# Optimization experiments

Measured on AMD Instinct MI355X. Metric: run time of the kernel, lower is better.

Reference implementation:

```python
import jax, jax.numpy as jnp
import numpy as np

N, T, H, L, E, F, CN, CG = 20000, 2, 128, 4, 320000, 514, 3, 2
EPS = 1e-7  # GENConv message epsilon


def _ln(x, g, b):
    mu = jnp.mean(x, axis=-1, keepdims=True)
    var = jnp.mean((x - mu) ** 2, axis=-1, keepdims=True)
    return (x - mu) / jnp.sqrt(var + 1e-5) * g + b


def _genconv(x, src, dst, e, W1, b1, g1, be1, W2, b2, t, n):
    # message: relu(x_j + edge_attr) + eps
    msg = jax.nn.relu(x[src] + e) + EPS  # [E,H]
    # softmax aggregation with learnable temperature t, grouped by dst
    logits = msg * t
    m = jax.ops.segment_max(logits, dst, num_segments=n)
    m = jnp.where(jnp.isfinite(m), m, 0.0)  # guard empty segments
    ex = jnp.exp(logits - m[dst])
    denom = jax.ops.segment_sum(ex, dst, num_segments=n)
    alpha = ex / (denom[dst] + 1e-16)
    agg = jax.ops.segment_sum(msg * alpha, dst, num_segments=n)  # [N,H]
    out = agg + x  # residual with root node (x_r)
    # MLP: Lin(H,2H) -> LayerNorm -> ReLU -> Lin(2H,H)
    h1 = jax.nn.relu(_ln(out @ W1 + b1, g1, be1))
    return h1 @ W2 + b2


def _attn(x, Wq, Wk, Wv, gamma):
    # x: [N, T, H]; channel (transform-axis) self-attention, gamma-gated residual
    q = jnp.einsum('tc,nch->nth', Wq, x)
    k = jnp.einsum('tc,nch->nth', Wk, x)
    v = jnp.einsum('tc,nch->nth', Wv, x)
    a = jax.nn.softmax(jnp.einsum('nth,nsh->nts', q, k), axis=-1)
    o = jnp.einsum('nts,nsh->nth', a, v)
    return gamma * o + x


def setup_inputs() -> dict:
    key = jax.random.key(0)
    ks = iter(jax.random.split(key, 48))

    def nrm(sh, s=0.02):
        return jax.random.normal(next(ks), sh, dtype=jnp.float32) * s

    inp = {}
    inp['node_feature'] = jax.random.normal(next(ks), (N, F), dtype=jnp.float32)
    inp['edge_index'] = jax.random.randint(next(ks), (T, 2, E), 0, N, dtype=jnp.int32)
    inp['edge_attr'] = jax.random.normal(next(ks), (T, E, 2), dtype=jnp.float32)
    # encoders
    inp['Wne'] = nrm((F, H)); inp['bne'] = jnp.zeros((H,), jnp.float32)
    inp['Wee'] = nrm((2, H)); inp['bee'] = jnp.zeros((H,), jnp.float32)
    # per-layer GENConv MLP params (stacked over L)
    inp['W1'] = nrm((L, H, 2 * H)); inp['b1'] = jnp.zeros((L, 2 * H), jnp.float32)
    inp['g1'] = jnp.ones((L, 2 * H), jnp.float32); inp['be1'] = jnp.zeros((L, 2 * H), jnp.float32)
    inp['W2'] = nrm((L, 2 * H, H)); inp['b2'] = jnp.zeros((L, H), jnp.float32)
    # DeepGCNLayer LayerNorms
    inp['dg'] = jnp.ones((L, H), jnp.float32); inp['db'] = jnp.zeros((L, H), jnp.float32)
    # learnable temperatures
    inp['t'] = jnp.ones((L,), jnp.float32)
    # node attention + head
    inp['Wq_n'] = nrm((T, T), 0.2); inp['Wk_n'] = nrm((T, T), 0.2); inp['Wv_n'] = nrm((T, T), 0.2)
    inp['gamma_n'] = jnp.float32(0.5)
    inp['Wn1'] = nrm((T * H, T * H)); inp['bn1'] = jnp.zeros((T * H,), jnp.float32)
    inp['Wn2'] = nrm((T * H, CN)); inp['bn2'] = jnp.zeros((CN,), jnp.float32)
    # graph attention + head
    inp['Wq_g'] = nrm((T, T), 0.2); inp['Wk_g'] = nrm((T, T), 0.2); inp['Wv_g'] = nrm((T, T), 0.2)
    inp['gamma_g'] = jnp.float32(0.5)
    inp['Wg1'] = nrm((T * H, T * H)); inp['bg1'] = jnp.zeros((T * H,), jnp.float32)
    inp['Wg2'] = nrm((T * H, CG)); inp['bg2'] = jnp.zeros((CG,), jnp.float32)
    return inp


def reference(node_feature, edge_index, edge_attr, Wne, bne, Wee, bee,
              W1, b1, g1, be1, W2, b2, dg, db, t,
              Wq_n, Wk_n, Wv_n, gamma_n, Wn1, bn1, Wn2, bn2,
              Wq_g, Wk_g, Wv_g, gamma_g, Wg1, bg1, Wg2, bg2):
    embs = []
    for ti in range(T):
        x = node_feature @ Wne + bne           # node_encoder
        e = edge_attr[ti] @ Wee + bee          # edge_encoder
        src, dst = edge_index[ti, 0], edge_index[ti, 1]
        # layers[0].conv applied directly
        x = _genconv(x, src, dst, e, W1[0], b1[0], g1[0], be1[0], W2[0], b2[0], t[0], N)
        # res+ DeepGCN blocks
        for l in range(1, L):
            h = jax.nn.relu(_ln(x, dg[l], db[l]))  # dropout p=0.1 is identity in eval
            x = x + _genconv(h, src, dst, e, W1[l], b1[l], g1[l], be1[l], W2[l], b2[l], t[l], N)
        x = jax.nn.relu(_ln(x, dg[0], db[0]))
        embs.append(x)
    emb = jnp.stack(embs, axis=1)  # [N, T, H]

    a = _attn(emb, Wq_n, Wk_n, Wv_n, gamma_n).reshape(N, T * H)
    node = jax.nn.relu(a @ Wn1 + bn1) @ Wn2 + bn2
    node = jax.nn.log_softmax(node, axis=-1)

    g = _attn(emb, Wq_g, Wk_g, Wv_g, gamma_g).reshape(N, T * H)
    gp = jnp.mean(g, axis=0, keepdims=True)  # global_mean_pool (single graph)
    gp = jax.nn.relu(gp @ Wg1 + bg1) @ Wg2 + bg2
    gp = jax.nn.log_softmax(gp, axis=-1)
    return (node, gp)
```

## Files before the change

kernel.cpp:

```cpp
#include <hip/hip_runtime.h>

#define NN 20000
#define TT 2
#define HH 128
#define LL 4
#define EE 320000
#define FF 514
#define CN 3
#define CG 2
#define EPS_MSG 1e-7f
#define MP 20096

typedef __bf16 bf16x8 __attribute__((ext_vector_type(8)));
typedef __bf16 bf16x4 __attribute__((ext_vector_type(4)));
typedef __bf16 bf16x2 __attribute__((ext_vector_type(2)));
typedef float f32x4 __attribute__((ext_vector_type(4)));

struct __align__(8) Edge { int src; __bf16 ea0, ea1; };

__device__ inline float wave_sum(float v) {
#pragma unroll
  for (int off = 32; off; off >>= 1) v += __shfl_xor(v, off);
  return v;
}
__device__ inline float red16(float v) {
  v += __shfl_xor(v, 1); v += __shfl_xor(v, 2);
  v += __shfl_xor(v, 4); v += __shfl_xor(v, 8);
  return v;
}

__device__ __forceinline__ void gload_lds16(const void* g, void* l) {
  __builtin_amdgcn_global_load_lds(
      (const __attribute__((address_space(1))) unsigned int*)g,
      (__attribute__((address_space(3))) unsigned int*)l, 16, 0, 0);
}

#define ENCB (MP / 64)
#define SCB 2500
#define CHUNK 5000
__global__ __launch_bounds__(256) void enc_scatter_kernel(
    const __bf16* __restrict__ A, const __bf16* __restrict__ BT,
    const float* __restrict__ bias, __bf16* __restrict__ C,
    const int* __restrict__ edge_index, const float* __restrict__ edge_attr,
    int* __restrict__ cursor, Edge* __restrict__ edges) {
  __shared__ __bf16 As[2][64][32];
  __shared__ __bf16 Bs[2][128][32];
  const int tid = threadIdx.x;
  if (blockIdx.x >= ENCB) {
    int chunk = blockIdx.x & 7;
    int i = ((blockIdx.x - ENCB) >> 3) * 256 + tid;
    if (i >= 2 * EE) return;
    int ti = (i >= EE) ? 1 : 0;
    int e = i - ti * EE;
    const int* srcp = edge_index + (size_t)ti * 2 * EE;
    int d = srcp[EE + e];
    int gnode = ti * NN + d;
    if (gnode / CHUNK != chunk) return;
    int s = srcp[e];
    float2 ea = ((const float2*)edge_attr)[(size_t)ti * EE + e];
    int pos = atomicAdd(&cursor[gnode], 1);
    Edge ed;
    ed.src = s + ti * MP;
    ed.ea0 = (__bf16)ea.x; ed.ea1 = (__bf16)ea.y;
    __builtin_memcpy(&edges[pos], &ed, sizeof(Edge));
    return;
  }
  const int K = 576;
  const int lane = tid & 63, w = tid >> 6;
  const int bm = blockIdx.x * 64;
  const int wr = (w >> 1) * 32, wc = (w & 1) * 64;
  const int fr = lane & 15, fq = lane >> 4;
  const int rowA = tid >> 2, chA = (tid & 3) * 8;
  const __bf16* Ab = A + (size_t)(bm + rowA) * K + chA;
  const __bf16* Bb = BT + (size_t)rowA * K + chA;
  const __bf16* Bb2 = Bb + (size_t)64 * K;
  f32x4 acc[2][4] = {};
#define STAGE(buf, k0)                                  \
  do {                                                  \
    gload_lds16(Ab + (k0), &As[buf][rowA][chA]);        \
    gload_lds16(Bb + (k0), &Bs[buf][rowA][chA]);        \
    gload_lds16(Bb2 + (k0), &Bs[buf][rowA + 64][chA]);  \
  } while (0)
  STAGE(0, 0);
  __syncthreads();
  int cur = 0;
  for (int k0 = 0; k0 < K; k0 += 32) {
    if (k0 + 32 < K) STAGE(cur ^ 1, k0 + 32);
    bf16x8 af[2], bq[4];
#pragma unroll
    for (int m = 0; m < 2; ++m)
      af[m] = *(const bf16x8*)&As[cur][wr + m * 16 + fr][fq * 8];
#pragma unroll
    for (int n = 0; n < 4; ++n)
      bq[n] = *(const bf16x8*)&Bs[cur][wc + n * 16 + fr][fq * 8];
#pragma unroll
    for (int m = 0; m < 2; ++m)
#pragma unroll
      for (int n = 0; n < 4; ++n)
        acc[m][n] =
            __builtin_amdgcn_mfma_f32_16x16x32_bf16(af[m], bq[n], acc[m][n], 0, 0, 0);
    __syncthreads();
    cur ^= 1;
  }
#undef STAGE
#pragma unroll
  for (int m = 0; m < 2; ++m) {
#pragma unroll
    for (int n = 0; n < 4; ++n) {
#pragma unroll
      for (int j = 0; j < 4; ++j) {
        int gm = bm + wr + m * 16 + fq * 4 + j;
        int gn = wc + n * 16 + fr;
        if (gm < NN) {
          __bf16 c = (__bf16)(acc[m][n][j] + bias[gn]);
          C[(size_t)gm * 128 + gn] = c;
          C[(size_t)(gm + MP) * 128 + gn] = c;
        }
      }
    }
  }
}

template <int EPI>
__global__ __launch_bounds__(256) void gemm256(
    const __bf16* __restrict__ A, const __bf16* __restrict__ BT,
    const float* __restrict__ bias, const float* __restrict__ g,
    const float* __restrict__ be, const float* __restrict__ W2h,
    const float* __restrict__ b2h, void* __restrict__ outp, int M, int K) {
  __shared__ __bf16 As[2][64][32];
  __shared__ __bf16 Bs[2][256][32];
  const int tid = threadIdx.x;
  const int lane = tid & 63, w = tid >> 6;
  const int bm = blockIdx.x * 64;
  const int wr = w * 16;
  const int fr = lane & 15, fq = lane >> 4;
  const int rowA = tid >> 2, chA = (tid & 3) * 8;
  const __bf16* Ab = A + (size_t)(bm + rowA) * K + chA;
  const __bf16* Bb = BT + (size_t)rowA * K + chA;
  f32x4 acc[16] = {};

#define STG(buf, k0)                                                \
  do {                                                              \
    gload_lds16(Ab + (k0), &As[buf][rowA][chA]);                    \
    _Pragma("unroll") for (int r = 0; r < 4; ++r)                   \
        gload_lds16(Bb + (size_t)(r * 64) * K + (k0),               \
                    &Bs[buf][rowA + r * 64][chA]);                  \
  } while (0)

  STG(0, 0);
  __syncthreads();
  int cur = 0;
  for (int k0 = 0; k0 < K; k0 += 32) {
    if (k0 + 32 < K) STG(cur ^ 1, k0 + 32);
    bf16x8 af = *(const bf16x8*)&As[cur][wr + fr][fq * 8];
#pragma unroll
    for (int n = 0; n < 16; ++n) {
      bf16x8 bq = *(const bf16x8*)&Bs[cur][n * 16 + fr][fq * 8];
      acc[n] = __builtin_amdgcn_mfma_f32_16x16x32_bf16(af, bq, acc[n], 0, 0, 0);
    }
    __syncthreads();
    cur ^= 1;
  }
#undef STG

  float cb[16];
#pragma unroll
  for (int n = 0; n < 16; ++n) cb[n] = bias[n * 16 + fr];

  if constexpr (EPI == 0) {
    float gv[16], bev[16];
#pragma unroll
    for (int n = 0; n < 16; ++n) {
      gv[n] = g[n * 16 + fr];
      bev[n] = be[n * 16 + fr];
    }
    __bf16* outb = (__bf16*)outp;
#pragma unroll
    for (int j = 0; j < 4; ++j) {
      float cj[16], s = 0.f, s2 = 0.f;
#pragma unroll
      for (int n = 0; n < 16; ++n) {
        float c = acc[n][j] + cb[n];
        cj[n] = c; s += c; s2 += c * c;
      }
      s = red16(s); s2 = red16(s2);
      float mu = s * (1.f / 256);
      float var = fmaxf(s2 * (1.f / 256) - mu * mu, 0.f);
      float rr = rsqrtf(var + 1e-5f);
      int gm = bm + wr + fq * 4 + j;
      __bf16* op = outb + (size_t)gm * 256;
#pragma unroll
      for (int n = 0; n < 16; ++n) {
        float y = (cj[n] - mu) * rr * gv[n] + bev[n];
        op[n * 16 + fr] = (__bf16)fmaxf(y, 0.f);
      }
    }
  } else {
    float w0[16], w1[16], w2[16];
#pragma unroll
    for (int n = 0; n < 16; ++n) {
      int col = n * 16 + fr;
      w0[n] = W2h[col * 3 + 0];
      w1[n] = W2h[col * 3 + 1];
      w2[n] = W2h[col * 3 + 2];
    }
    float* outf = (float*)outp;
#pragma unroll
    for (int j = 0; j < 4; ++j) {
      float p0 = 0.f, p1 = 0.f, p2 = 0.f;
#pragma unroll
      for (int n = 0; n < 16; ++n) {
        float h = fmaxf(acc[n][j] + cb[n], 0.f);
        p0 += h * w0[n]; p1 += h * w1[n]; p2 += h * w2[n];
      }
      p0 = red16(p0); p1 = red16(p1); p2 = red16(p2);
      int gm = bm + wr + fq * 4 + j;
      if (fr == 0 && gm < M) {
        float l0 = p0 + b2h[0], l1 = p1 + b2h[1], l2 = p2 + b2h[2];
        float m = fmaxf(l0, fmaxf(l1, l2));
        float lse = m + logf(__expf(l0 - m) + __expf(l1 - m) + __expf(l2 - m));
        outf[(size_t)gm * 3 + 0] = l0 - lse;
        outf[(size_t)gm * 3 + 1] = l1 - lse;
        outf[(size_t)gm * 3 + 2] = l2 - lse;
      }
    }
  }
}

template <int MODE>
__global__ __launch_bounds__(256) void gemm_lin2(
    const __bf16* __restrict__ A, const __bf16* __restrict__ BT,
    const float* __restrict__ bias, float* __restrict__ xres,
    const float* __restrict__ g, const float* __restrict__ be,
    void* __restrict__ lnout) {
  __shared__ __bf16 As[2][64][32];
  __shared__ __bf16 Bs[2][128][32];
  __shared__ float redS[64][2], redS2[64][2];
  const int tid = threadIdx.x;
  const int lane = tid & 63, w = tid >> 6;
  const int bm = blockIdx.x * 64;
  const int wr = (w >> 1) * 32, wc = (w & 1) * 64;
  const int fr = lane & 15, fq = lane >> 4;
  const int rowA = tid >> 2, chA = (tid & 3) * 8;
  const __bf16* Ab = A + (size_t)(bm + rowA) * 256 + chA;
  const __bf16* Bb = BT + (size_t)rowA * 256 + chA;
  const __bf16* Bb2 = Bb + (size_t)64 * 256;
  f32x4 acc[2][4] = {};

#define STAGE(buf, k0)                                  \
  do {                                                  \
    gload_lds16(Ab + (k0), &As[buf][rowA][chA]);        \
    gload_lds16(Bb + (k0), &Bs[buf][rowA][chA]);        \
    gload_lds16(Bb2 + (k0), &Bs[buf][rowA + 64][chA]);  \
  } while (0)

  STAGE(0, 0);
  __syncthreads();
  int cur = 0;
  for (int k0 = 0; k0 < 256; k0 += 32) {
    if (k0 + 32 < 256) STAGE(cur ^ 1, k0 + 32);
    bf16x8 af[2], bq[4];
#pragma unroll
    for (int m = 0; m < 2; ++m)
      af[m] = *(const bf16x8*)&As[cur][wr + m * 16 + fr][fq * 8];
#pragma unroll
    for (int n = 0; n < 4; ++n)
      bq[n] = *(const bf16x8*)&Bs[cur][wc + n * 16 + fr][fq * 8];
#pragma unroll
    for (int m = 0; m < 2; ++m)
#pragma unroll
      for (int n = 0; n < 4; ++n)
        acc[m][n] =
            __builtin_amdgcn_mfma_f32_16x16x32_bf16(af[m], bq[n], acc[m][n], 0, 0, 0);
    __syncthreads();
    cur ^= 1;
  }
#undef STAGE

  float cv[2][4][4];
#pragma unroll
  for (int m = 0; m < 2; ++m) {
    int r0 = wr + m * 16 + fq * 4;
#pragma unroll
    for (int j = 0; j < 4; ++j) {
      int gm = bm + r0 + j;
      float s = 0.f, s2 = 0.f;
#pragma unroll
      for (int n = 0; n < 4; ++n) {
        float c = acc[m][n][j] + bias[wc + n * 16 + fr];
        if (MODE != 0) c += xres[(size_t)gm * 128 + wc + n * 16 + fr];
        cv[m][n][j] = c;
        s += c; s2 += c * c;
      }
      s = red16(s); s2 = red16(s2);
      if (fr == 0) {
        redS[r0 + j][w & 1] = s;
        redS2[r0 + j][w & 1] = s2;
      }
    }
  }
  __syncthreads();
#pragma unroll
  for (int m = 0; m < 2; ++m) {
    int r0 = wr + m * 16 + fq * 4;
#pragma unroll
    for (int j = 0; j < 4; ++j) {
      int r = r0 + j;
      int gm = bm + r;
      float S = redS[r][0] + redS[r][1];
      float S2 = redS2[r][0] + redS2[r][1];
      float mu = S * (1.f / 128);
      float var = fmaxf(S2 * (1.f / 128) - mu * mu, 0.f);
      float rr = rsqrtf(var + 1e-5f);
      if constexpr (MODE < 2) {
        float* xp = xres + (size_t)gm * 128;
        __bf16* hp = (__bf16*)lnout + (size_t)gm * 128;
#pragma unroll
        for (int n = 0; n < 4; ++n) {
          int col = wc + n * 16 + fr;
          float c = cv[m][n][j];
          xp[col] = c;
          float y = (c - mu) * rr * g[col] + be[col];
          hp[col] = (__bf16)fmaxf(y, 0.f);
        }
      } else {
        int half = gm >= MP;
        int node = gm - half * MP;
        if (node < NN) {
          float* ep = (float*)lnout + (size_t)node * 256 + half * 128;
#pragma unroll
          for (int n = 0; n < 4; ++n) {
            int col = wc + n * 16 + fr;
            float y = (cv[m][n][j] - mu) * rr * g[col] + be[col];
            ep[col] = fmaxf(y, 0.f);
          }
        }
      }
    }
  }
}

struct WtDesc { const float* src; __bf16* dst; int K, N, Kpad; };
struct WtDescs { WtDesc d[10]; };
#define NF2B 20079
#define PADB 2422
#define WTB 2880
#define CNTB 2500

__global__ void prep_kernel(const float* __restrict__ nf_src,
                            __bf16* __restrict__ nf_dst, WtDescs descs,
                            const int* __restrict__ edge_index,
                            int* __restrict__ deg, float* __restrict__ gp_sum) {
  int b = blockIdx.x, tid = threadIdx.x;
  if (b < NF2B) {
    int i = b * 256 + tid;
    if (i >= NN * FF / 2) return;
    int row = i / 257;
    int col = (i - row * 257) * 2;
    float2 v = ((const float2*)nf_src)[i];
    bf16x2 o; o[0] = (__bf16)v.x; o[1] = (__bf16)v.y;
    *(bf16x2*)(nf_dst + (size_t)row * 576 + col) = o;
  } else if (b < NF2B + PADB) {
    int i = (b - NF2B) * 256 + tid;
    if (i >= NN * 31) return;
    int row = i / 31, j = i - row * 31;
    bf16x2 z; z[0] = (__bf16)0.f; z[1] = (__bf16)0.f;
    *(bf16x2*)(nf_dst + (size_t)row * 576 + 514 + 2 * j) = z;
  } else if (b < NF2B + PADB + WTB) {
    int wb = b - NF2B - PADB;
    WtDesc de = descs.d[wb / 288];
    int idx = (wb % 288) * 256 + tid;
    if (idx >= de.N * de.Kpad) return;
    int n = idx / de.Kpad, k = idx - n * de.Kpad;
    float v = (k < de.K) ? de.src[(size_t)k * de.N + n] : 0.f;
    de.dst[idx] = (__bf16)v;
  } else if (b < NF2B + PADB + WTB + CNTB) {
    int i = (b - NF2B - PADB - WTB) * 256 + tid;
    if (i >= 2 * EE) return;
    int ti = (i >= EE) ? 1 : 0;
    int e = i - ti * EE;
    int d = edge_index[(size_t)ti * 2 * EE + EE + e];
    atomicAdd(&deg[ti * NN + d], 1);
  } else {
    gp_sum[tid] = 0.f;
  }
}

__global__ __launch_bounds__(1024) void scan2_kernel(
    const int* __restrict__ deg_all, int* __restrict__ rowptr,
    int* __restrict__ cursor) {
  const int ti = blockIdx.x;
  const int* deg = deg_all + ti * NN;
  __shared__ int sums[1024];
  int tid = threadIdx.x;
  int chunk = (NN + 1023) / 1024;
  int begin = tid * chunk, end = min(begin + chunk, NN);
  int s = 0;
  for (int i = begin; i < end; ++i) s += deg[i];
  sums[tid] = s;
  __syncthreads();
  for (int off = 1; off < 1024; off <<= 1) {
    int v = (tid >= off) ? sums[tid - off] : 0;
    __syncthreads();
    sums[tid] += v;
    __syncthreads();
  }
  int running = ti * EE + sums[tid] - s;
  for (int i = begin; i < end; ++i) {
    rowptr[ti * NN + i] = running;
    cursor[ti * NN + i] = running;
    running += deg[i];
  }
  if (tid == 0 && ti == 1) rowptr[2 * NN] = 2 * EE;
}

__global__ __launch_bounds__(256) void agg_kernel(
    const __bf16* __restrict__ xin, const int* __restrict__ rowptr,
    const Edge* __restrict__ edges, const float* __restrict__ Wee,
    const float* __restrict__ bee, const float* __restrict__ tptr, int layer,
    __bf16* __restrict__ out) {
  int wave = threadIdx.x >> 6, lane = threadIdx.x & 63;
  int b = blockIdx.x;
  int h8 = b & 7;
  int half = h8 >> 2;
  int within = (b >> 3) * 4 + (h8 & 3);
  int node = within * 4 + wave;
  int gnode = half * NN + node;
  int xrow = half * MP + node;
  float t = tptr[layer];
  int hh = lane >> 5, c32 = lane & 31, c0 = c32 * 4;
  float w0[4], w1[4], bv[4];
#pragma unroll
  for (int i = 0; i < 4; ++i) {
    w0[i] = Wee[c0 + i];
    w1[i] = Wee[HH + c0 + i];
    bv[i] = bee[c0 + i];
  }
  float den[4] = {}, num[4] = {};
  int e = rowptr[gnode], e1 = rowptr[gnode + 1];

#define MLP4(XV, ED)                                                \
  do {                                                              \
    float eax = (float)(ED).ea0, eay = (float)(ED).ea1;             \
    _Pragma("unroll") for (int i = 0; i < 4; ++i) {                 \
      float m = (float)(XV)[i] + eax * w0[i] + eay * w1[i] + bv[i]; \
      m = fmaxf(m, 0.f) + EPS_MSG;                                  \
      float ex = __expf(m * t);                                     \
      den[i] += ex; num[i] += m * ex;                               \
    }                                                               \
  } while (0)

  for (; e + 8 <= e1; e += 8) {
    Edge E0 = edges[e + hh], E1 = edges[e + 2 + hh];
    Edge E2 = edges[e + 4 + hh], E3 = edges[e + 6 + hh];
    bf16x4 x0 = *(const bf16x4*)(xin + (size_t)E0.src * HH + c0);
    bf16x4 x1 = *(const bf16x4*)(xin + (size_t)E1.src * HH + c0);
    bf16x4 x2 = *(const bf16x4*)(xin + (size_t)E2.src * HH + c0);
    bf16x4 x3 = *(const bf16x4*)(xin + (size_t)E3.src * HH + c0);
    MLP4(x0, E0); MLP4(x1, E1); MLP4(x2, E2); MLP4(x3, E3);
  }
  if (e + 4 <= e1) {
    Edge E0 = edges[e + hh], E1 = edges[e + 2 + hh];
    bf16x4 x0 = *(const bf16x4*)(xin + (size_t)E0.src * HH + c0);
    bf16x4 x1 = *(const bf16x4*)(xin + (size_t)E1.src * HH + c0);
    MLP4(x0, E0); MLP4(x1, E1);
    e += 4;
  }
  if (e + hh < e1) {
    Edge Ea = edges[e + hh];
    bf16x4 xa = *(const bf16x4*)(xin + (size_t)Ea.src * HH + c0);
    MLP4(xa, Ea);
  }
  if (e + 2 + hh < e1) {
    Edge Ea = edges[e + 2 + hh];
    bf16x4 xa = *(const bf16x4*)(xin + (size_t)Ea.src * HH + c0);
    MLP4(xa, Ea);
  }
#undef MLP4

#pragma unroll
  for (int i = 0; i < 4; ++i) {
    den[i] += __shfl_xor(den[i], 32);
    num[i] += __shfl_xor(num[i], 32);
  }
  if (hh == 0) {
    bf16x4 xr = *(const bf16x4*)(xin + (size_t)xrow * HH + c0);
    bf16x4 o;
#pragma unroll
    for (int i = 0; i < 4; ++i)
      o[i] = (__bf16)(num[i] / (den[i] + 1e-16f) + (float)xr[i]);
    *(bf16x4*)(out + (size_t)xrow * HH + c0) = o;
  }
}

__global__ __launch_bounds__(256) void attn2_kernel(
    const float* __restrict__ emb, const float* __restrict__ Wq_n,
    const float* __restrict__ Wk_n, const float* __restrict__ Wv_n,
    const float* __restrict__ gn, const float* __restrict__ Wq_g,
    const float* __restrict__ Wk_g, const float* __restrict__ Wv_g,
    const float* __restrict__ gg, __bf16* __restrict__ outn,
    float* __restrict__ outg, int nNodes) {
  int wave = threadIdx.x >> 6, lane = threadIdx.x & 63;
  int n = blockIdx.x * 4 + wave;
  if (n >= nNodes) return;
  int c0 = lane * 2;
  const float* base = emb + (size_t)n * (2 * HH);
  float2 x0 = *(const float2*)(base + c0);
  float2 x1 = *(const float2*)(base + HH + c0);

#define ATTN_BODY(Wq, Wk, Wv, GAM, O0A, O0B, O1A, O1B)                        \
  {                                                                           \
    float gamma = *(GAM);                                                     \
    float wq00 = Wq[0], wq01 = Wq[1], wq10 = Wq[2], wq11 = Wq[3];             \
    float wk00 = Wk[0], wk01 = Wk[1], wk10 = Wk[2], wk11 = Wk[3];             \
    float wv00 = Wv[0], wv01 = Wv[1], wv10 = Wv[2], wv11 = Wv[3];             \
    float q0a = wq00 * x0.x + wq01 * x1.x, q0b = wq00 * x0.y + wq01 * x1.y;   \
    float q1a = wq10 * x0.x + wq11 * x1.x, q1b = wq10 * x0.y + wq11 * x1.y;   \
    float k0a = wk00 * x0.x + wk01 * x1.x, k0b = wk00 * x0.y + wk01 * x1.y;   \
    float k1a = wk10 * x0.x + wk11 * x1.x, k1b = wk10 * x0.y + wk11 * x1.y;   \
    float v0a = wv00 * x0.x + wv01 * x1.x, v0b = wv00 * x0.y + wv01 * x1.y;   \
    float v1a = wv10 * x0.x + wv11 * x1.x, v1b = wv10 * x0.y + wv11 * x1.y;   \
    float s00 = wave_sum(q0a * k0a + q0b * k0b);                              \
    float s01 = wave_sum(q0a * k1a + q0b * k1b);                              \
    float s10 = wave_sum(q1a * k0a + q1b * k0b);                              \
    float s11 = wave_sum(q1a * k1a + q1b * k1b);                              \
    float m0 = fmaxf(s00, s01);                                               \
    float e00 = __expf(s00 - m0), e01 = __expf(s01 - m0);                     \
    float i0 = 1.f / (e00 + e01);                                             \
    float a00 = e00 * i0, a01 = e01 * i0;                                     \
    float m1 = fmaxf(s10, s11);                                               \
    float e10 = __expf(s10 - m1), e11 = __expf(s11 - m1);                     \
    float i1 = 1.f / (e10 + e11);                                             \
    float a10 = e10 * i1, a11 = e11 * i1;                                     \
    O0A = gamma * (a00 * v0a + a01 * v1a) + x0.x;                             \
    O0B = gamma * (a00 * v0b + a01 * v1b) + x0.y;                             \
    O1A = gamma * (a10 * v0a + a11 * v1a) + x1.x;                             \
    O1B = gamma * (a10 * v0b + a11 * v1b) + x1.y;                             \
  }

  float n0a, n0b, n1a, n1b;
  ATTN_BODY(Wq_n, Wk_n, Wv_n, gn, n0a, n0b, n1a, n1b);
  __bf16* opn = outn + (size_t)n * (2 * HH);
  bf16x2 t0; t0[0] = (__bf16)n0a; t0[1] = (__bf16)n0b;
  bf16x2 t1; t1[0] = (__bf16)n1a; t1[1] = (__bf16)n1b;
  *(bf16x2*)(opn + c0) = t0;
  *(bf16x2*)(opn + HH + c0) = t1;

  float g0a, g0b, g1a, g1b;
  ATTN_BODY(Wq_g, Wk_g, Wv_g, gg, g0a, g0b, g1a, g1b);
  float* opg = outg + (size_t)n * (2 * HH);
  *(float2*)(opg + c0) = make_float2(g0a, g0b);
  *(float2*)(opg + HH + c0) = make_float2(g1a, g1b);
#undef ATTN_BODY
}

__global__ __launch_bounds__(256) void pool_kernel(const float* __restrict__ gbuf,
                                                   float* __restrict__ gp_sum, int nNodes) {
  int c = threadIdx.x;
  float s = 0.f;
  for (int r = blockIdx.x; r < nNodes; r += gridDim.x) s += gbuf[(size_t)r * 256 + c];
  atomicAdd(&gp_sum[c], s);
}

__global__ __launch_bounds__(256) void graph_head_kernel(
    const float* __restrict__ gp_sum, const float* __restrict__ Wg1,
    const float* __restrict__ bg1, const float* __restrict__ Wg2,
    const float* __restrict__ bg2, float* __restrict__ outp, float invN) {
  __shared__ float gp[256];
  __shared__ float h1[256];
  __shared__ float lg[2];
  int tid = threadIdx.x;
  gp[tid] = gp_sum[tid] * invN;
  __syncthreads();
  float acc = bg1[tid];
  for (int k = 0; k < 256; ++k) acc += gp[k] * Wg1[k * 256 + tid];
  h1[tid] = fmaxf(acc, 0.f);
  __syncthreads();
  if (tid < 2) {
    float l = bg2[tid];
    for (int c = 0; c < 256; ++c) l += h1[c] * Wg2[c * 2 + tid];
    lg[tid] = l;
  }
  __syncthreads();
  if (tid == 0) {
    float m = fmaxf(lg[0], lg[1]);
    float lse = m + logf(__expf(lg[0] - m) + __expf(lg[1] - m));
    outp[0] = lg[0] - lse;
    outp[1] = lg[1] - lse;
  }
}

extern "C" void kernel_launch(void* const* d_in, const int* in_sizes, int n_in,
                              void* d_out, int out_size, void* d_ws, size_t ws_size,
                              hipStream_t stream) {
  (void)in_sizes; (void)n_in; (void)out_size; (void)ws_size;
  const float* node_feature = (const float*)d_in[0];
  const int* edge_index = (const int*)d_in[1];
  const float* edge_attr = (const float*)d_in[2];
  const float* Wne = (const float*)d_in[3];
  const float* bne = (const float*)d_in[4];
  const float* Wee = (const float*)d_in[5];
  const float* bee = (const float*)d_in[6];
  const float* W1 = (const float*)d_in[7];
  const float* b1 = (const float*)d_in[8];
  const float* g1 = (const float*)d_in[9];
  const float* be1 = (const float*)d_in[10];
  const float* W2 = (const float*)d_in[11];
  const float* b2 = (const float*)d_in[12];
  const float* dg = (const float*)d_in[13];
  const float* db = (const float*)d_in[14];
  const float* tpar = (const float*)d_in[15];
  const float* Wq_n = (const float*)d_in[16];
  const float* Wk_n = (const float*)d_in[17];
  const float* Wv_n = (const float*)d_in[18];
  const float* gamma_n = (const float*)d_in[19];
  const float* Wn1 = (const float*)d_in[20];
  const float* bn1 = (const float*)d_in[21];
  const float* Wn2 = (const float*)d_in[22];
  const float* bn2 = (const float*)d_in[23];
  const float* Wq_g = (const float*)d_in[24];
  const float* Wk_g = (const float*)d_in[25];
  const float* Wv_g = (const float*)d_in[26];
  const float* gamma_g = (const float*)d_in[27];
  const float* Wg1 = (const float*)d_in[28];
  const float* bg1 = (const float*)d_in[29];
  const float* Wg2 = (const float*)d_in[30];
  const float* bg2 = (const float*)d_in[31];
  float* out = (float*)d_out;

  char* pc = (char*)d_ws;
  auto alloc = [&](size_t bytes) {
    char* r = pc;
    pc += (bytes + 255) & ~(size_t)255;
    return r;
  };
  float* xbuf = (float*)alloc((size_t)2 * MP * HH * 4);
  __bf16* hbuf_b = (__bf16*)alloc((size_t)2 * MP * HH * 2);
  __bf16* t256_b = (__bf16*)alloc((size_t)2 * MP * 256 * 2);
  float* emb = (float*)alloc((size_t)NN * 2 * HH * 4);
  __bf16* aggout_b = (__bf16*)alloc((size_t)2 * MP * HH * 2);
  __bf16* nf_b = (__bf16*)emb;
  __bf16* attnb = t256_b;
  float* buf2 = xbuf;
  __bf16* wt_ne = (__bf16*)alloc((size_t)128 * 576 * 2);
  __bf16* wt1 = (__bf16*)alloc((size_t)4 * 256 * 128 * 2);
  __bf16* wt2 = (__bf16*)alloc((size_t)4 * 128 * 256 * 2);
  __bf16* wtn1 = (__bf16*)alloc((size_t)256 * 256 * 2);
  float* gp_sum = (float*)alloc(256 * 4);
  int* deg = (int*)alloc((size_t)2 * NN * 4);
  int* cursor = (int*)alloc((size_t)2 * NN * 4);
  int* rowptr = (int*)alloc((size_t)(2 * NN + 2) * 4);
  Edge* edges = (Edge*)alloc((size_t)2 * EE * 8);

  const int gRows2 = 2 * MP / 64;

  WtDescs wd;
  wd.d[0] = {Wne, wt_ne, FF, HH, 576};
  for (int l = 0; l < 4; ++l)
    wd.d[1 + l] = {W1 + (size_t)l * HH * 256, wt1 + (size_t)l * 256 * HH, HH, 256, HH};
  for (int l = 0; l < 4; ++l)
    wd.d[5 + l] = {W2 + (size_t)l * 256 * HH, wt2 + (size_t)l * HH * 256, 256, HH, 256};
  wd.d[9] = {Wn1, wtn1, 256, 256, 256};

  hipMemsetAsync(deg, 0, 2 * NN * sizeof(int), stream);
  prep_kernel<<<NF2B + PADB + WTB + CNTB + 1, 256, 0, stream>>>(
      node_feature, nf_b, wd, edge_index, deg, gp_sum);
  scan2_kernel<<<2, 1024, 0, stream>>>(deg, rowptr, cursor);
  enc_scatter_kernel<<<ENCB + 8 * SCB, 256, 0, stream>>>(
      nf_b, wt_ne, bne, hbuf_b, edge_index, edge_attr, cursor, edges);

  for (int l = 0; l < LL; ++l) {
    agg_kernel<<<2 * NN / 4, 256, 0, stream>>>(hbuf_b, rowptr, edges, Wee, bee, tpar,
                                               l, aggout_b);
    gemm256<0><<<gRows2, 256, 0, stream>>>(aggout_b, wt1 + (size_t)l * 256 * HH,
                                           b1 + l * 2 * HH, g1 + l * 2 * HH,
                                           be1 + l * 2 * HH, nullptr, nullptr, t256_b,
                                           2 * MP, HH);
    const __bf16* w2l = wt2 + (size_t)l * HH * 256;
    const float* b2l = b2 + l * HH;
    if (l == 0)
      gemm_lin2<0><<<gRows2, 256, 0, stream>>>(t256_b, w2l, b2l, xbuf, dg + 1 * HH,
                                               db + 1 * HH, hbuf_b);
    else if (l < LL - 1)
      gemm_lin2<1><<<gRows2, 256, 0, stream>>>(t256_b, w2l, b2l, xbuf,
                                               dg + (l + 1) * HH, db + (l + 1) * HH,
                                               hbuf_b);
    else
      gemm_lin2<2><<<gRows2, 256, 0, stream>>>(t256_b, w2l, b2l, xbuf, dg, db, emb);
  }

  attn2_kernel<<<(NN + 3) / 4, 256, 0, stream>>>(emb, Wq_n, Wk_n, Wv_n, gamma_n,
                                                 Wq_g, Wk_g, Wv_g, gamma_g, attnb,
                                                 buf2, NN);
  gemm256<1><<<MP / 64, 256, 0, stream>>>(attnb, wtn1, bn1, nullptr, nullptr, Wn2,
                                          bn2, out, NN, 256);
  pool_kernel<<<128, 256, 0, stream>>>(buf2, gp_sum, NN);
  graph_head_kernel<<<1, 256, 0, stream>>>(gp_sum, Wg1, bg1, Wg2, bg2,
                                           out + (size_t)NN * CN, 1.0f / NN);
}
```

Baseline: 511.8 us.

## Split agg channels across blocks, use exp2, pre-reduce graph pool in attention

The aggregation kernel now gives each block one half of the 128 channels of its node. Each wave covers 64 channels with 16 lanes and handles 4 edges at a time, which doubles the grid and the number of wave-level edge loads. The softmax exponential switches to a native exp2 with the temperature pre-scaled by log2(e). The attention kernel also reduces the graph-branch output over each block's 4 nodes in LDS and writes only per-block partial sums, so the full per-node float buffer is never written and pool_kernel reads a quarter of the rows. The cost is more edge-index reads, since each edge list is walked by two blocks, and the removed bounds check relies on NN being divisible by 4.

```diff
diff --git a/kernel.cpp b/kernel.cpp
--- a/kernel.cpp
+++ b/kernel.cpp
@@ -27,6 +27,14 @@
   v += __shfl_xor(v, 1); v += __shfl_xor(v, 2);
   v += __shfl_xor(v, 4); v += __shfl_xor(v, 8);
   return v;
+}
+
+__device__ __forceinline__ float fexp2(float x) {
+#if __has_builtin(__builtin_amdgcn_exp2f)
+  return __builtin_amdgcn_exp2f(x);
+#else
+  return exp2f(x);
+#endif
 }
 
 __device__ __forceinline__ void gload_lds16(const void* g, void* l) {
@@ -421,14 +429,17 @@
     __bf16* __restrict__ out) {
   int wave = threadIdx.x >> 6, lane = threadIdx.x & 63;
   int b = blockIdx.x;
-  int h8 = b & 7;
-  int half = h8 >> 2;
-  int within = (b >> 3) * 4 + (h8 & 3);
-  int node = within * 4 + wave;
-  int gnode = half * NN + node;
-  int xrow = half * MP + node;
-  float t = tptr[layer];
-  int hh = lane >> 5, c32 = lane & 31, c0 = c32 * 4;
+  int x8 = b & 7;
+  int q = x8 >> 1;
+  int par = x8 & 1;
+  int ti = q >> 1, chh = q & 1;
+  int group = (b >> 3) * 2 + par;
+  int node = group * 4 + wave;
+  int gnode = ti * NN + node;
+  int xrow = ti * MP + node;
+  float t2 = tptr[layer] * 1.4426950408889634f;
+  int qq = lane >> 4, c15 = lane & 15;
+  int c0 = chh * 64 + c15 * 4;
   float w0[4], w1[4], bv[4];
 #pragma unroll
   for (int i = 0; i < 4; ++i) {
@@ -445,45 +456,39 @@
     _Pragma("unroll") for (int i = 0; i < 4; ++i) {                 \
       float m = (float)(XV)[i] + eax * w0[i] + eay * w1[i] + bv[i]; \
       m = fmaxf(m, 0.f) + EPS_MSG;                                  \
-      float ex = __expf(m * t);                                     \
+      float ex = fexp2(m * t2);                                     \
       den[i] += ex; num[i] += m * ex;                               \
     }                                                               \
   } while (0)
 
   for (; e + 8 <= e1; e += 8) {
-    Edge E0 = edges[e + hh], E1 = edges[e + 2 + hh];
-    Edge E2 = edges[e + 4 + hh], E3 = edges[e + 6 + hh];
+    Edge E0 = edges[e + qq];
+    Edge E1 = edges[e + 4 + qq];
     bf16x4 x0 = *(const bf16x4*)(xin + (size_t)E0.src * HH + c0);
     bf16x4 x1 = *(const bf16x4*)(xin + (size_t)E1.src * HH + c0);
-    bf16x4 x2 = *(const bf16x4*)(xin + (size_t)E2.src * HH + c0);
-    bf16x4 x3 = *(const bf16x4*)(xin + (size_t)E3.src * HH + c0);
-    MLP4(x0, E0); MLP4(x1, E1); MLP4(x2, E2); MLP4(x3, E3);
-  }
-  if (e + 4 <= e1) {
-    Edge E0 = edges[e + hh], E1 = edges[e + 2 + hh];
+    MLP4(x0, E0);
+    MLP4(x1, E1);
+  }
+  if (e + qq < e1) {
+    Edge E0 = edges[e + qq];
     bf16x4 x0 = *(const bf16x4*)(xin + (size_t)E0.src * HH + c0);
-    bf16x4 x1 = *(const bf16x4*)(xin + (size_t)E1.src * HH + c0);
-    MLP4(x0, E0); MLP4(x1, E1);
-    e += 4;
-  }
-  if (e + hh < e1) {
-    Edge Ea = edges[e + hh];
-    bf16x4 xa = *(const bf16x4*)(xin + (size_t)Ea.src * HH + c0);
-    MLP4(xa, Ea);
-  }
-  if (e + 2 + hh < e1) {
-    Edge Ea = edges[e + 2 + hh];
-    bf16x4 xa = *(const bf16x4*)(xin + (size_t)Ea.src * HH + c0);
-    MLP4(xa, Ea);
+    MLP4(x0, E0);
+  }
+  if (e + 4 + qq < e1) {
+    Edge E0 = edges[e + 4 + qq];
+    bf16x4 x0 = *(const bf16x4*)(xin + (size_t)E0.src * HH + c0);
+    MLP4(x0, E0);
   }
 #undef MLP4
 
 #pragma unroll
   for (int i = 0; i < 4; ++i) {
+    den[i] += __shfl_xor(den[i], 16);
     den[i] += __shfl_xor(den[i], 32);
+    num[i] += __shfl_xor(num[i], 16);
     num[i] += __shfl_xor(num[i], 32);
   }
-  if (hh == 0) {
+  if (qq == 0) {
     bf16x4 xr = *(const bf16x4*)(xin + (size_t)xrow * HH + c0);
     bf16x4 o;
 #pragma unroll
@@ -499,10 +504,11 @@
     const float* __restrict__ gn, const float* __restrict__ Wq_g,
     const float* __restrict__ Wk_g, const float* __restrict__ Wv_g,
     const float* __restrict__ gg, __bf16* __restrict__ outn,
-    float* __restrict__ outg, int nNodes) {
+    float* __restrict__ partial) {
+  __shared__ float gsum[4][256];
   int wave = threadIdx.x >> 6, lane = threadIdx.x & 63;
+  int tid = threadIdx.x;
   int n = blockIdx.x * 4 + wave;
-  if (n >= nNodes) return;
   int c0 = lane * 2;
   const float* base = emb + (size_t)n * (2 * HH);
   float2 x0 = *(const float2*)(base + c0);
@@ -548,17 +554,23 @@
 
   float g0a, g0b, g1a, g1b;
   ATTN_BODY(Wq_g, Wk_g, Wv_g, gg, g0a, g0b, g1a, g1b);
-  float* opg = outg + (size_t)n * (2 * HH);
-  *(float2*)(opg + c0) = make_float2(g0a, g0b);
-  *(float2*)(opg + HH + c0) = make_float2(g1a, g1b);
+  gsum[wave][c0] = g0a;
+  gsum[wave][c0 + 1] = g0b;
+  gsum[wave][128 + c0] = g1a;
+  gsum[wave][129 + c0] = g1b;
+  __syncthreads();
+  partial[(size_t)blockIdx.x * 256 + tid] =
+      gsum[0][tid] + gsum[1][tid] + gsum[2][tid] + gsum[3][tid];
 #undef ATTN_BODY
 }
 
-__global__ __launch_bounds__(256) void pool_kernel(const float* __restrict__ gbuf,
-                                                   float* __restrict__ gp_sum, int nNodes) {
+__global__ __launch_bounds__(256) void pool_kernel(const float* __restrict__ partial,
+                                                   float* __restrict__ gp_sum,
+                                                   int nRows) {
   int c = threadIdx.x;
   float s = 0.f;
-  for (int r = blockIdx.x; r < nNodes; r += gridDim.x) s += gbuf[(size_t)r * 256 + c];
+  for (int r = blockIdx.x; r < nRows; r += gridDim.x)
+    s += partial[(size_t)r * 256 + c];
   atomicAdd(&gp_sum[c], s);
 }
 
@@ -641,7 +653,7 @@
   __bf16* aggout_b = (__bf16*)alloc((size_t)2 * MP * HH * 2);
   __bf16* nf_b = (__bf16*)emb;
   __bf16* attnb = t256_b;
-  float* buf2 = xbuf;
+  float* partial = xbuf;
   __bf16* wt_ne = (__bf16*)alloc((size_t)128 * 576 * 2);
   __bf16* wt1 = (__bf16*)alloc((size_t)4 * 256 * 128 * 2);
   __bf16* wt2 = (__bf16*)alloc((size_t)4 * 128 * 256 * 2);
@@ -670,8 +682,8 @@
       nf_b, wt_ne, bne, hbuf_b, edge_index, edge_attr, cursor, edges);
 
   for (int l = 0; l < LL; ++l) {
-    agg_kernel<<<2 * NN / 4, 256, 0, stream>>>(hbuf_b, rowptr, edges, Wee, bee, tpar,
-                                               l, aggout_b);
+    agg_kernel<<<2500 * 8, 256, 0, stream>>>(hbuf_b, rowptr, edges, Wee, bee, tpar,
+                                             l, aggout_b);
     gemm256<0><<<gRows2, 256, 0, stream>>>(aggout_b, wt1 + (size_t)l * 256 * HH,
                                            b1 + l * 2 * HH, g1 + l * 2 * HH,
                                            be1 + l * 2 * HH, nullptr, nullptr, t256_b,
@@ -689,12 +701,11 @@
       gemm_lin2<2><<<gRows2, 256, 0, stream>>>(t256_b, w2l, b2l, xbuf, dg, db, emb);
   }
 
-  attn2_kernel<<<(NN + 3) / 4, 256, 0, stream>>>(emb, Wq_n, Wk_n, Wv_n, gamma_n,
-                                                 Wq_g, Wk_g, Wv_g, gamma_g, attnb,
-                                                 buf2, NN);
+  attn2_kernel<<<NN / 4, 256, 0, stream>>>(emb, Wq_n, Wk_n, Wv_n, gamma_n, Wq_g,
+                                           Wk_g, Wv_g, gamma_g, attnb, partial);
   gemm256<1><<<MP / 64, 256, 0, stream>>>(attnb, wtn1, bn1, nullptr, nullptr, Wn2,
                                           bn2, out, NN, 256);
-  pool_kernel<<<128, 256, 0, stream>>>(buf2, gp_sum, NN);
+  pool_kernel<<<128, 256, 0, stream>>>(partial, gp_sum, NN / 4);
   graph_head_kernel<<<1, 256, 0, stream>>>(gp_sum, Wg1, bg1, Wg2, bg2,
                                            out + (size_t)NN * CN, 1.0f / NN);
 }
```

After: 487.9 us. 4.7% less time.
